# Performance work log

Measured on AMD Instinct MI355X. Metric: run time of the kernel, lower is better.

## Reference

```python
import jax, jax.numpy as jnp
import numpy as np

S, B, V = 128, 64, 32000
EH, EO, H, O = 512, 512, 1024, 1024
THRESH = 1e-06


def _thresh(x):
    # nn.Threshold(1e-6, 0): x if x > 1e-6 else 0
    return jnp.where(x > THRESH, x, 0.0)


def setup_inputs() -> dict:
    key = jax.random.key(0)
    ks = jax.random.split(key, 12)
    ids = jax.random.randint(ks[0], (S, B), 0, V, dtype=jnp.int32)
    s = 0.02
    return {
        "ids": ids,
        "W1": jax.random.normal(ks[1], (EH, V), jnp.float32) * s,
        "b1": jax.random.normal(ks[2], (EH,), jnp.float32) * s,
        "W2": jax.random.normal(ks[3], (EO, EH), jnp.float32) * s,
        "b2": jax.random.normal(ks[4], (EO,), jnp.float32) * s,
        "W_ih": jax.random.normal(ks[5], (3 * H, EO), jnp.float32) * s,
        "b_ih": jax.random.normal(ks[6], (3 * H,), jnp.float32) * s,
        "W_hh": jax.random.normal(ks[7], (3 * H, H), jnp.float32) * s,
        "b_hh": jax.random.normal(ks[8], (3 * H,), jnp.float32) * s,
        "W_out": jax.random.normal(ks[9], (O, H), jnp.float32) * s,
        "b_out": jax.random.normal(ks[10], (O,), jnp.float32) * s,
    }


def reference(ids, W1, b1, W2, b2, W_ih, b_ih, W_hh, b_hh, W_out, b_out):
    # one_hot(ids, V) @ W1.T + b1 == exact gather of W1 columns (sum of zeros is exact)
    emb = _thresh(jnp.take(W1.T, ids, axis=0) + b1)            # [S, B, EH]
    x = _thresh(jnp.einsum('sbe,oe->sbo', emb, W2) + b2)       # [S, B, EO]
    # Precompute all input-gate projections in one GEMM
    xW = jnp.einsum('sbe,ge->sbg', x, W_ih) + b_ih             # [S, B, 3H]

    def step(h, xw):
        gh = h @ W_hh.T + b_hh                                 # [B, 3H]
        xr, xz, xn = jnp.split(xw, 3, axis=-1)
        hr, hz, hn = jnp.split(gh, 3, axis=-1)
        r = jax.nn.sigmoid(xr + hr)
        z = jax.nn.sigmoid(xz + hz)
        n = jnp.tanh(xn + r * hn)
        h_new = (1.0 - z) * n + z * h
        return h_new, None

    h0 = jnp.zeros((B, H), dtype=x.dtype)
    hT, _ = jax.lax.scan(step, h0, xW)                         # [B, H]
    # Dropout is identity in inference; final Linear
    out = hT @ W_out.T + b_out                                 # [B, O]
    return out[None]                                           # [1, B, O] (h_n layout)
```

## Files before the change

### kernel.cpp

```cpp
#include <hip/hip_runtime.h>
#include <stdint.h>
#include <stddef.h>

#define S_LEN 128
#define B_SZ  64
#define V_SZ  32000
#define EH    512
#define EO    512
#define H_SZ  1024
#define O_SZ  1024
#define G3    3072

typedef __attribute__((ext_vector_type(8))) short short8;
typedef __attribute__((ext_vector_type(4))) float floatx4;
typedef __attribute__((ext_vector_type(8))) unsigned short ushortx8;
typedef __attribute__((ext_vector_type(4))) unsigned uintx4;

__device__ __forceinline__ unsigned short f2bf(float f) {
  unsigned u = __builtin_bit_cast(unsigned, f);
  u += 0x7FFFu + ((u >> 16) & 1u);
  return (unsigned short)(u >> 16);
}
__device__ __forceinline__ float bf2f(unsigned short h) {
  unsigned u = ((unsigned)h) << 16;
  return __builtin_bit_cast(float, u);
}

__device__ __forceinline__ void gld_lds16(const void* g, void* l) {
  __builtin_amdgcn_global_load_lds((const __attribute__((address_space(1))) void*)g,
                                   (__attribute__((address_space(3))) void*)l, 16, 0, 0);
}

__global__ __launch_bounds__(256) void cvt2_bf16(const float* __restrict__ a,
                                                 const float* __restrict__ b,
                                                 unsigned short* __restrict__ out) {
  const int na4 = (EO * EH) / 4;
  int i = blockIdx.x * 256 + threadIdx.x;
  const float* src;
  int off;
  if (i < na4) { src = a; off = i; }
  else         { src = b; off = i - na4; }
  float4 v = ((const float4*)src)[off];
  ushort4 o;
  o.x = f2bf(v.x); o.y = f2bf(v.y); o.z = f2bf(v.z); o.w = f2bf(v.w);
  ((ushort4*)out)[i] = o;
}

__global__ __launch_bounds__(256) void transpose_w1_bf16(const float* __restrict__ W1,
                                                         unsigned short* __restrict__ W1T) {
  __shared__ unsigned short tile[64][72];
  int t = threadIdx.x;
  int v0 = blockIdx.x * 64;
  int e0 = blockIdx.y * 64;
  for (int i = 0; i < 4; ++i) {
    int e = (t >> 4) + i * 16;
    int v = (t & 15) * 4;
    float4 w = *(const float4*)&W1[(size_t)(e0 + e) * V_SZ + v0 + v];
    tile[v + 0][e] = f2bf(w.x);
    tile[v + 1][e] = f2bf(w.y);
    tile[v + 2][e] = f2bf(w.z);
    tile[v + 3][e] = f2bf(w.w);
  }
  __syncthreads();
  for (int i = 0; i < 2; ++i) {
    int v = (t >> 3) + i * 32;
    int e = (t & 7) * 8;
    ushortx8 o;
    for (int j = 0; j < 8; ++j) o[j] = tile[v][e + j];
    *(ushortx8*)&W1T[(size_t)(v0 + v) * EH + e0 + e] = o;
  }
}

__global__ __launch_bounds__(256) void gather_emb(const int* __restrict__ ids,
                                                  const unsigned short* __restrict__ W1T,
                                                  const float* __restrict__ b1,
                                                  unsigned short* __restrict__ emb) {
  int t = threadIdx.x;
  int tok = blockIdx.x * 4 + (t >> 6);
  int lane = t & 63;
  int id = ids[tok];
  ushortx8 w = *(const ushortx8*)&W1T[(size_t)id * EH + lane * 8];
  float4 blo = *(const float4*)&b1[lane * 8];
  float4 bhi = *(const float4*)&b1[lane * 8 + 4];
  float bv[8] = {blo.x, blo.y, blo.z, blo.w, bhi.x, bhi.y, bhi.z, bhi.w};
  ushortx8 o;
  for (int j = 0; j < 8; ++j) {
    float x = bf2f(w[j]) + bv[j];
    x = (x > 1e-6f) ? x : 0.0f;
    o[j] = f2bf(x);
  }
  *(ushortx8*)&emb[(size_t)tok * EH + lane * 8] = o;
}

template <int ACT, int OUT_BF16>
__global__ __launch_bounds__(256) void gemm_bt(const unsigned short* __restrict__ A,
                                               const unsigned short* __restrict__ B,
                                               const float* __restrict__ bias,
                                               void* __restrict__ Cout,
                                               int M, int N, int K) {
  __shared__ unsigned short lA[128 * 64];
  __shared__ unsigned short lB[128 * 64];
  int t = threadIdx.x;
  int lane = t & 63;
  int wave = t >> 6;
  int bn = blockIdx.x, bm = blockIdx.y;
  int wm = (wave >> 1) * 64;
  int wn = (wave & 1) * 64;
  floatx4 acc[4][4] = {};

  int srow = t >> 3;
  int sslot = (t & 7) ^ (srow & 7);
  int scol = sslot * 8;

  const unsigned short* aptr[4];
  const unsigned short* bptr[4];
#pragma unroll
  for (int p = 0; p < 4; ++p) {
    int gra = bm * 128 + p * 32 + srow;  if (gra >= M) gra = M - 1;
    aptr[p] = A + (size_t)gra * K + scol;
    bptr[p] = B + (size_t)(bn * 128 + p * 32 + srow) * K + scol;
  }

  for (int k0 = 0; k0 < K; k0 += 64) {
    __syncthreads();
#pragma unroll
    for (int p = 0; p < 4; ++p) {
      gld_lds16(aptr[p] + k0, &lA[p * 2048 + t * 8]);
      gld_lds16(bptr[p] + k0, &lB[p * 2048 + t * 8]);
    }
    __syncthreads();
#pragma unroll
    for (int kk = 0; kk < 2; ++kk) {
      short8 af[4], bfr[4];
#pragma unroll
      for (int i = 0; i < 4; ++i) {
        int row = wm + i * 16 + (lane & 15);
        int phys = (kk * 4 + (lane >> 4)) ^ (row & 7);
        af[i] = *(const short8*)&lA[row * 64 + phys * 8];
      }
#pragma unroll
      for (int j = 0; j < 4; ++j) {
        int row = wn + j * 16 + (lane & 15);
        int phys = (kk * 4 + (lane >> 4)) ^ (row & 7);
        bfr[j] = *(const short8*)&lB[row * 64 + phys * 8];
      }
#pragma unroll
      for (int i = 0; i < 4; ++i)
#pragma unroll
        for (int j = 0; j < 4; ++j)
          acc[i][j] = __builtin_amdgcn_mfma_f32_16x16x32_bf16(af[i], bfr[j], acc[i][j], 0, 0, 0);
    }
  }

  int rowq = (lane >> 4) * 4;
  for (int j = 0; j < 4; ++j) {
    int col = bn * 128 + wn + j * 16 + (lane & 15);
    float bv = bias[col];
    for (int i = 0; i < 4; ++i) {
      int row0 = bm * 128 + wm + i * 16 + rowq;
      for (int r = 0; r < 4; ++r) {
        int row = row0 + r;
        if (row < M) {
          float v = acc[i][j][r] + bv;
          if (ACT) v = (v > 1e-6f) ? v : 0.0f;
          if (OUT_BF16) ((unsigned short*)Cout)[(size_t)row * N + col] = f2bf(v);
          else          ((float*)Cout)[(size_t)row * N + col] = v;
        }
      }
    }
  }
}

__global__ __launch_bounds__(256) void prep_whh(const float* __restrict__ W_hh,
                                                unsigned short* __restrict__ Wprep) {
  int tid = blockIdx.x * 256 + threadIdx.x;
  int lane = tid & 63;
  int c = tid >> 6;
  int cg = c / 96;
  int r  = c % 96;
  int g  = r >> 5;
  int t  = r & 31;
  int row = g * H_SZ + cg * 16 + (lane & 15);
  int k   = t * 32 + (lane >> 4) * 8;
  const float* src = &W_hh[(size_t)row * H_SZ + k];
  float4 v0 = *(const float4*)src;
  float4 v1 = *(const float4*)(src + 4);
  ushortx8 o;
  o[0] = f2bf(v0.x); o[1] = f2bf(v0.y); o[2] = f2bf(v0.z); o[3] = f2bf(v0.w);
  o[4] = f2bf(v1.x); o[5] = f2bf(v1.y); o[6] = f2bf(v1.z); o[7] = f2bf(v1.w);
  ((ushortx8*)Wprep)[tid] = o;
}

__global__ __launch_bounds__(256) void prep_wih(const float* __restrict__ W_ih,
                                                unsigned short* __restrict__ Wihp) {
  int tid = blockIdx.x * 256 + threadIdx.x;
  int lane = tid & 63;
  int c = tid >> 6;
  int cg = c / 48;
  int r  = c % 48;
  int g  = r >> 4;
  int kq = r & 15;
  int row = g * H_SZ + cg * 16 + (lane & 15);
  int k   = kq * 32 + (lane >> 4) * 8;
  const float* src = &W_ih[(size_t)row * EO + k];
  float4 v0 = *(const float4*)src;
  float4 v1 = *(const float4*)(src + 4);
  ushortx8 o;
  o[0] = f2bf(v0.x); o[1] = f2bf(v0.y); o[2] = f2bf(v0.z); o[3] = f2bf(v0.w);
  o[4] = f2bf(v1.x); o[5] = f2bf(v1.y); o[6] = f2bf(v1.z); o[7] = f2bf(v1.w);
  ((ushortx8*)Wihp)[tid] = o;
}

__global__ __launch_bounds__(256) void gru_persist(const unsigned short* __restrict__ hprep0,
                                                   unsigned short* __restrict__ hprep1,
                                                   unsigned short* __restrict__ hbfinal,
                                                   const unsigned short* __restrict__ Wprep,
                                                   const unsigned short* __restrict__ Wihp,
                                                   const float* __restrict__ b_hh,
                                                   const float* __restrict__ b_ih,
                                                   const unsigned short* __restrict__ x,
                                                   unsigned* __restrict__ bar) {
  __shared__ unsigned short lB[96 * 512];
  __shared__ unsigned short lWih[48 * 512];
  __shared__ float lgh[3][4][256];
  __shared__ float lgx[3][256];
  int t = threadIdx.x;
  int lane = t & 63;
  int w = t >> 6;
  int bg = blockIdx.x >> 6;
  int cg = blockIdx.x & 63;

  const unsigned short* wsrc = Wprep + (size_t)cg * 96 * 512;
  for (int i = 0; i < 24; ++i) {
    int c = w * 24 + i;
    gld_lds16(wsrc + (size_t)c * 512 + lane * 8, &lB[c * 512 + lane * 8]);
  }
  const unsigned short* wxs = Wihp + (size_t)cg * 48 * 512;
  for (int i = 0; i < 12; ++i) {
    int c = w * 12 + i;
    gld_lds16(wxs + (size_t)c * 512 + lane * 8, &lWih[c * 512 + lane * 8]);
  }

  int b_loc = t >> 4;
  int j_loc = t & 15;
  int jcol = cg * 16 + j_loc;
  int bglob = bg * 16 + b_loc;
  float bhr = b_hh[jcol];
  float bhz = b_hh[H_SZ + jcol];
  float bhn = b_hh[2 * H_SZ + jcol];
  float bihr = b_ih[jcol];
  float bihz = b_ih[H_SZ + jcol];
  float bihn = b_ih[2 * H_SZ + jcol];
  int tt2 = jcol >> 5;
  int q   = (jcol >> 3) & 3;
  int jj  = jcol & 7;
  int Ls  = b_loc | (q << 4);
  size_t hw_off32 = ((((size_t)(bg * 32 + tt2) * 64 + Ls) * 8) + (jj & ~1)) >> 1;

  const unsigned short* hbufs[2] = {hprep0, hprep1};
  unsigned* barp = bar + bg * 64;
  float hmaster = 0.0f;

  auto xw_compute = [&](int sn) {
    int g = w - 1;
    const unsigned short* xrow =
        x + ((size_t)(sn * B_SZ + bg * 16 + (lane & 15))) * EO + (lane >> 4) * 8;
    floatx4 accx = {};
#pragma unroll
    for (int kq = 0; kq < 16; ++kq) {
      uintx4 xv = *(const uintx4*)(xrow + kq * 32);
      short8 a = __builtin_bit_cast(short8, xv);
      short8 bfr = *(const short8*)&lWih[((g * 16 + kq) * 64 + lane) * 8];
      accx = __builtin_amdgcn_mfma_f32_16x16x32_bf16(a, bfr, accx, 0, 0, 0);
    }
#pragma unroll
    for (int r = 0; r < 4; ++r)
      lgx[g][((lane >> 4) * 4 + r) * 16 + (lane & 15)] = accx[r];
  };

  __syncthreads();

  if (w >= 1) xw_compute(0);
  __syncthreads();
  float xr = lgx[0][t] + bihr;
  float xz = lgx[1][t] + bihz;
  float xn = lgx[2][t] + bihn;

  for (int s = 0; s < S_LEN; ++s) {
    const unsigned short* hr = hbufs[s & 1];
    unsigned* hw32 = (unsigned*)hbufs[(s + 1) & 1];

    uintx4 av[8];
#pragma unroll
    for (int i = 0; i < 8; ++i) {
      int tt = w * 8 + i;
      const void* ap = hr + ((size_t)(bg * 32 + tt) * 64 + lane) * 8;
      asm volatile("global_load_dwordx4 %0, %1, off sc1" : "=v"(av[i]) : "v"(ap));
    }
    asm volatile("s_waitcnt vmcnt(0)"
                 : "+v"(av[0]), "+v"(av[1]), "+v"(av[2]), "+v"(av[3]),
                   "+v"(av[4]), "+v"(av[5]), "+v"(av[6]), "+v"(av[7])
                 :: "memory");

    floatx4 acc[3] = {};
#pragma unroll
    for (int i = 0; i < 8; ++i) {
      int tt = w * 8 + i;
      short8 a = __builtin_bit_cast(short8, av[i]);
#pragma unroll
      for (int g = 0; g < 3; ++g) {
        short8 bfr = *(const short8*)&lB[((g * 32 + tt) * 64 + lane) * 8];
        acc[g] = __builtin_amdgcn_mfma_f32_16x16x32_bf16(a, bfr, acc[g], 0, 0, 0);
      }
    }
#pragma unroll
    for (int g = 0; g < 3; ++g)
#pragma unroll
      for (int r = 0; r < 4; ++r)
        lgh[g][w][((lane >> 4) * 4 + r) * 16 + (lane & 15)] = acc[g][r];
    __syncthreads();

    float ghr = lgh[0][0][t] + lgh[0][1][t] + lgh[0][2][t] + lgh[0][3][t] + bhr;
    float ghz = lgh[1][0][t] + lgh[1][1][t] + lgh[1][2][t] + lgh[1][3][t] + bhz;
    float ghn = lgh[2][0][t] + lgh[2][1][t] + lgh[2][2][t] + lgh[2][3][t] + bhn;
    float rr = 1.0f / (1.0f + __expf(-(xr + ghr)));
    float zz = 1.0f / (1.0f + __expf(-(xz + ghz)));
    float nn = tanhf(xn + rr * ghn);
    float hnew = (1.0f - zz) * nn + zz * hmaster;
    hmaster = hnew;

    unsigned hb = (unsigned)f2bf(hnew);
    unsigned other = (unsigned)__shfl_xor((int)hb, 1);
    if ((jj & 1) == 0) {
      unsigned packed = hb | (other << 16);
      __hip_atomic_store(hw32 + hw_off32, packed,
                         __ATOMIC_RELAXED, __HIP_MEMORY_SCOPE_AGENT);
    }
    if (s == S_LEN - 1) hbfinal[(size_t)bglob * H_SZ + jcol] = (unsigned short)hb;

    if (s < S_LEN - 1) {
      __syncthreads();
      if (w == 0) {
        if (t == 0) {
          __hip_atomic_fetch_add(barp, 1u, __ATOMIC_RELAXED, __HIP_MEMORY_SCOPE_AGENT);
          unsigned target = 64u * (unsigned)(s + 1);
          while (__hip_atomic_load(barp, __ATOMIC_RELAXED, __HIP_MEMORY_SCOPE_AGENT) < target)
            __builtin_amdgcn_s_sleep(2);
        }
      } else {
        xw_compute(s + 1);
      }
      __syncthreads();
      xr = lgx[0][t] + bihr;
      xz = lgx[1][t] + bihz;
      xn = lgx[2][t] + bihn;
    }
  }
}

extern "C" void kernel_launch(void* const* d_in, const int* in_sizes, int n_in,
                              void* d_out, int out_size, void* d_ws, size_t ws_size,
                              hipStream_t stream) {
  const int*   ids   = (const int*)d_in[0];
  const float* W1    = (const float*)d_in[1];
  const float* b1    = (const float*)d_in[2];
  const float* W2    = (const float*)d_in[3];
  const float* b2    = (const float*)d_in[4];
  const float* W_ih  = (const float*)d_in[5];
  const float* b_ih  = (const float*)d_in[6];
  const float* W_hh  = (const float*)d_in[7];
  const float* b_hh  = (const float*)d_in[8];
  const float* W_out = (const float*)d_in[9];
  const float* b_out = (const float*)d_in[10];
  float* out = (float*)d_out;

  uint8_t* wsp = (uint8_t*)d_ws;
  auto alloc = [&](size_t bytes) {
    uint8_t* p = wsp;
    wsp += (bytes + 255) & ~(size_t)255;
    return p;
  };
  unsigned short* W1T   = (unsigned short*)alloc((size_t)V_SZ * EH * 2);
  unsigned short* W2b   = (unsigned short*)alloc((size_t)EO * EH * 2);
  unsigned short* Woutb = (unsigned short*)alloc((size_t)O_SZ * H_SZ * 2);
  unsigned short* Wprep = (unsigned short*)alloc((size_t)G3 * H_SZ * 2);
  unsigned short* Wihp  = (unsigned short*)alloc((size_t)G3 * EO * 2);
  unsigned short* emb   = (unsigned short*)alloc((size_t)S_LEN * B_SZ * EH * 2);
  unsigned short* x     = (unsigned short*)alloc((size_t)S_LEN * B_SZ * EO * 2);
  unsigned short* hprep0 = (unsigned short*)alloc((size_t)B_SZ * H_SZ * 2);
  unsigned short* hprep1 = (unsigned short*)alloc((size_t)B_SZ * H_SZ * 2);
  unsigned short* hbfinal = (unsigned short*)alloc((size_t)B_SZ * H_SZ * 2);
  unsigned*       bar     = (unsigned*)alloc(1024);

  cvt2_bf16<<<dim3(1280), 256, 0, stream>>>(W2, W_out, W2b);

  prep_whh<<<dim3(1536), 256, 0, stream>>>(W_hh, Wprep);
  prep_wih<<<dim3(768), 256, 0, stream>>>(W_ih, Wihp);

  hipMemsetAsync(hprep0, 0, (size_t)B_SZ * H_SZ * 2, stream);
  hipMemsetAsync(bar, 0, 1024, stream);

  transpose_w1_bf16<<<dim3(V_SZ / 64, EH / 64), 256, 0, stream>>>(W1, W1T);

  gather_emb<<<dim3(S_LEN * B_SZ / 4), 256, 0, stream>>>(ids, W1T, b1, emb);

  gemm_bt<1, 1><<<dim3(EO / 128, S_LEN * B_SZ / 128), 256, 0, stream>>>(
      emb, W2b, b2, x, S_LEN * B_SZ, EO, EH);

  {
    void* args[] = {(void*)&hprep0, (void*)&hprep1, (void*)&hbfinal,
                    (void*)&Wprep, (void*)&Wihp, (void*)&b_hh, (void*)&b_ih,
                    (void*)&x, (void*)&bar};
    hipLaunchCooperativeKernel((const void*)gru_persist, dim3(256), dim3(256),
                               args, 0, stream);
  }

  gemm_bt<0, 0><<<dim3(O_SZ / 128, 1), 256, 0, stream>>>(
      hbfinal, Woutb, b_out, out, B_SZ, O_SZ, H_SZ);
}
```

Before: 699.0 us.

## Fuse input projection into recurrent MFMA loop and prefetch next x

The per-step input-gate projection no longer runs in waves 1-3 during the barrier wait. Each wave now handles a K-slice of the x·W_ih product inside the same accumulators as the h·W_hh MFMAs for the r and z gates, with a separate accumulator for the n gate. The next step's x rows are prefetched into registers right after use, so their load overlaps the barrier. This spreads the x work across all four waves and removes the extra LDS round trip for r and z, at the cost of more MFMAs on the critical path between barriers. Launch bounds are also set to one block per CU.

```diff
diff --git a/kernel.cpp b/kernel.cpp
--- a/kernel.cpp
+++ b/kernel.cpp
@@ -211,19 +211,19 @@
   ((ushortx8*)Wihp)[tid] = o;
 }
 
-__global__ __launch_bounds__(256) void gru_persist(const unsigned short* __restrict__ hprep0,
-                                                   unsigned short* __restrict__ hprep1,
-                                                   unsigned short* __restrict__ hbfinal,
-                                                   const unsigned short* __restrict__ Wprep,
-                                                   const unsigned short* __restrict__ Wihp,
-                                                   const float* __restrict__ b_hh,
-                                                   const float* __restrict__ b_ih,
-                                                   const unsigned short* __restrict__ x,
-                                                   unsigned* __restrict__ bar) {
+__global__ __launch_bounds__(256, 1) void gru_persist(const unsigned short* __restrict__ hprep0,
+                                                      unsigned short* __restrict__ hprep1,
+                                                      unsigned short* __restrict__ hbfinal,
+                                                      const unsigned short* __restrict__ Wprep,
+                                                      const unsigned short* __restrict__ Wihp,
+                                                      const float* __restrict__ b_hh,
+                                                      const float* __restrict__ b_ih,
+                                                      const unsigned short* __restrict__ x,
+                                                      unsigned* __restrict__ bar) {
   __shared__ unsigned short lB[96 * 512];
   __shared__ unsigned short lWih[48 * 512];
   __shared__ float lgh[3][4][256];
-  __shared__ float lgx[3][256];
+  __shared__ float lgxn[4][256];
   int t = threadIdx.x;
   int lane = t & 63;
   int w = t >> 6;
@@ -245,11 +245,9 @@
   int j_loc = t & 15;
   int jcol = cg * 16 + j_loc;
   int bglob = bg * 16 + b_loc;
-  float bhr = b_hh[jcol];
-  float bhz = b_hh[H_SZ + jcol];
-  float bhn = b_hh[2 * H_SZ + jcol];
-  float bihr = b_ih[jcol];
-  float bihz = b_ih[H_SZ + jcol];
+  float brz_r = b_hh[jcol] + b_ih[jcol];
+  float brz_z = b_hh[H_SZ + jcol] + b_ih[H_SZ + jcol];
+  float bhn  = b_hh[2 * H_SZ + jcol];
   float bihn = b_ih[2 * H_SZ + jcol];
   int tt2 = jcol >> 5;
   int q   = (jcol >> 3) & 3;
@@ -261,30 +259,15 @@
   unsigned* barp = bar + bg * 64;
   float hmaster = 0.0f;
 
-  auto xw_compute = [&](int sn) {
-    int g = w - 1;
-    const unsigned short* xrow =
-        x + ((size_t)(sn * B_SZ + bg * 16 + (lane & 15))) * EO + (lane >> 4) * 8;
-    floatx4 accx = {};
-#pragma unroll
-    for (int kq = 0; kq < 16; ++kq) {
-      uintx4 xv = *(const uintx4*)(xrow + kq * 32);
-      short8 a = __builtin_bit_cast(short8, xv);
-      short8 bfr = *(const short8*)&lWih[((g * 16 + kq) * 64 + lane) * 8];
-      accx = __builtin_amdgcn_mfma_f32_16x16x32_bf16(a, bfr, accx, 0, 0, 0);
-    }
-#pragma unroll
-    for (int r = 0; r < 4; ++r)
-      lgx[g][((lane >> 4) * 4 + r) * 16 + (lane & 15)] = accx[r];
-  };
+  const unsigned short* xbase =
+      x + ((size_t)(bg * 16 + (lane & 15))) * EO + (lane >> 4) * 8 + (w * 4) * 32;
 
   __syncthreads();
 
-  if (w >= 1) xw_compute(0);
-  __syncthreads();
-  float xr = lgx[0][t] + bihr;
-  float xz = lgx[1][t] + bihz;
-  float xn = lgx[2][t] + bihn;
+  uintx4 xf[4];
+#pragma unroll
+  for (int i = 0; i < 4; ++i)
+    asm volatile("global_load_dwordx4 %0, %1, off" : "=v"(xf[i]) : "v"(xbase + i * 32));
 
   for (int s = 0; s < S_LEN; ++s) {
     const unsigned short* hr = hbufs[s & 1];
@@ -299,10 +282,12 @@
     }
     asm volatile("s_waitcnt vmcnt(0)"
                  : "+v"(av[0]), "+v"(av[1]), "+v"(av[2]), "+v"(av[3]),
-                   "+v"(av[4]), "+v"(av[5]), "+v"(av[6]), "+v"(av[7])
+                   "+v"(av[4]), "+v"(av[5]), "+v"(av[6]), "+v"(av[7]),
+                   "+v"(xf[0]), "+v"(xf[1]), "+v"(xf[2]), "+v"(xf[3])
                  :: "memory");
 
     floatx4 acc[3] = {};
+    floatx4 accn = {};
 #pragma unroll
     for (int i = 0; i < 8; ++i) {
       int tt = w * 8 + i;
@@ -314,18 +299,41 @@
       }
     }
 #pragma unroll
+    for (int i = 0; i < 4; ++i) {
+      int kq = w * 4 + i;
+      short8 a = __builtin_bit_cast(short8, xf[i]);
+      short8 b0 = *(const short8*)&lWih[((0 * 16 + kq) * 64 + lane) * 8];
+      short8 b1 = *(const short8*)&lWih[((1 * 16 + kq) * 64 + lane) * 8];
+      short8 b2 = *(const short8*)&lWih[((2 * 16 + kq) * 64 + lane) * 8];
+      acc[0] = __builtin_amdgcn_mfma_f32_16x16x32_bf16(a, b0, acc[0], 0, 0, 0);
+      acc[1] = __builtin_amdgcn_mfma_f32_16x16x32_bf16(a, b1, acc[1], 0, 0, 0);
+      accn   = __builtin_amdgcn_mfma_f32_16x16x32_bf16(a, b2, accn,   0, 0, 0);
+    }
+
+    if (s + 1 < S_LEN) {
+      const unsigned short* xrow = xbase + (size_t)(s + 1) * B_SZ * EO;
+#pragma unroll
+      for (int i = 0; i < 4; ++i)
+        asm volatile("global_load_dwordx4 %0, %1, off" : "=v"(xf[i]) : "v"(xrow + i * 32));
+    }
+
+#pragma unroll
     for (int g = 0; g < 3; ++g)
 #pragma unroll
       for (int r = 0; r < 4; ++r)
         lgh[g][w][((lane >> 4) * 4 + r) * 16 + (lane & 15)] = acc[g][r];
+#pragma unroll
+    for (int r = 0; r < 4; ++r)
+      lgxn[w][((lane >> 4) * 4 + r) * 16 + (lane & 15)] = accn[r];
     __syncthreads();
 
-    float ghr = lgh[0][0][t] + lgh[0][1][t] + lgh[0][2][t] + lgh[0][3][t] + bhr;
-    float ghz = lgh[1][0][t] + lgh[1][1][t] + lgh[1][2][t] + lgh[1][3][t] + bhz;
+    float grs = lgh[0][0][t] + lgh[0][1][t] + lgh[0][2][t] + lgh[0][3][t] + brz_r;
+    float gzs = lgh[1][0][t] + lgh[1][1][t] + lgh[1][2][t] + lgh[1][3][t] + brz_z;
     float ghn = lgh[2][0][t] + lgh[2][1][t] + lgh[2][2][t] + lgh[2][3][t] + bhn;
-    float rr = 1.0f / (1.0f + __expf(-(xr + ghr)));
-    float zz = 1.0f / (1.0f + __expf(-(xz + ghz)));
-    float nn = tanhf(xn + rr * ghn);
+    float xnv = lgxn[0][t] + lgxn[1][t] + lgxn[2][t] + lgxn[3][t] + bihn;
+    float rr = 1.0f / (1.0f + __expf(-grs));
+    float zz = 1.0f / (1.0f + __expf(-gzs));
+    float nn = tanhf(xnv + rr * ghn);
     float hnew = (1.0f - zz) * nn + zz * hmaster;
     hmaster = hnew;
 
@@ -340,20 +348,13 @@
 
     if (s < S_LEN - 1) {
       __syncthreads();
-      if (w == 0) {
-        if (t == 0) {
-          __hip_atomic_fetch_add(barp, 1u, __ATOMIC_RELAXED, __HIP_MEMORY_SCOPE_AGENT);
-          unsigned target = 64u * (unsigned)(s + 1);
-          while (__hip_atomic_load(barp, __ATOMIC_RELAXED, __HIP_MEMORY_SCOPE_AGENT) < target)
-            __builtin_amdgcn_s_sleep(2);
-        }
-      } else {
-        xw_compute(s + 1);
+      if (t == 0) {
+        __hip_atomic_fetch_add(barp, 1u, __ATOMIC_RELAXED, __HIP_MEMORY_SCOPE_AGENT);
+        unsigned target = 64u * (unsigned)(s + 1);
+        while (__hip_atomic_load(barp, __ATOMIC_RELAXED, __HIP_MEMORY_SCOPE_AGENT) < target)
+          __builtin_amdgcn_s_sleep(2);
       }
       __syncthreads();
-      xr = lgx[0][t] + bihr;
-      xz = lgx[1][t] + bihz;
-      xn = lgx[2][t] + bihn;
     }
   }
 }
```

Measured after the change: 621.0 us. 11.2% less time.
